# Kernel optimization log

Hardware: AMD Instinct MI355X
Metric: run time of the kernel (lower is better)

Reference implementation:

```python
import jax, jax.numpy as jnp
import numpy as np
from jax import lax

B, C, O, K, L, W = 32, 128, 128, 3, 4096, 1
PAD, DIL = 1, 1


def _conv(x, w, b):
    # x: [B,C,H,W], w: [O,C,K,1] -> [B,O,H,W] (zeros padding, stride 1)
    y = lax.conv_general_dilated(x, w, window_strides=(1, 1),
                                 padding=[(PAD, PAD), (0, 0)],
                                 rhs_dilation=(DIL, 1),
                                 dimension_numbers=('NCHW', 'OIHW', 'NCHW'))
    return y + b[None, :, None, None]


def setup_inputs() -> dict:
    key = jax.random.key(0)
    ks = jax.random.split(key, 6)
    x = jax.random.normal(ks[0], (B, C, L, W), dtype=jnp.float32)
    # offset/modulator convs are zero-init in torch; use small random values to
    # exercise the deformable gather path (represents a trained state)
    w_off = jax.random.normal(ks[1], (2 * K, C, K, 1), dtype=jnp.float32) * 0.01
    b_off = jax.random.normal(ks[2], (2 * K,), dtype=jnp.float32) * 0.1
    w_mod = jax.random.normal(ks[3], (K, C, K, 1), dtype=jnp.float32) * 0.01
    b_mod = jax.random.normal(ks[4], (K,), dtype=jnp.float32) * 0.1
    w_reg = jax.random.normal(ks[5], (O, C, K, 1), dtype=jnp.float32) * (1.0 / np.sqrt(C * K))
    return {"x": x, "w_off": w_off, "b_off": b_off,
            "w_mod": w_mod, "b_mod": b_mod, "w_reg": w_reg}


def reference(x, w_off, b_off, w_mod, b_mod, w_reg):
    b, c, h, w = x.shape
    max_offset = max(h, w) / 4.0
    offset = jnp.clip(_conv(x, w_off, b_off), -max_offset, max_offset)  # [B,2K,H,W]
    mask = 2.0 * jax.nn.sigmoid(_conv(x, w_mod, b_mod))                 # [B,K,H,W]

    off = offset.reshape(b, K, 2, h, w)
    off_y, off_x = off[:, :, 0], off[:, :, 1]                           # [B,K,H,W]

    # sampling positions (stride=1, pad_w=0, kw=1)
    base_y = (-PAD + jnp.arange(K, dtype=jnp.float32)[:, None] * DIL
              + jnp.arange(h, dtype=jnp.float32)[None, :])              # [K,H]
    py = base_y[None, :, :, None] + off_y                               # [B,K,H,W]
    px = jnp.arange(w, dtype=jnp.float32)[None, None, None, :] + off_x  # [B,K,H,W]

    y0 = jnp.floor(py); x0 = jnp.floor(px)
    iy0 = y0.astype(jnp.int32); ix0 = x0.astype(jnp.int32)
    wy1 = py - y0; wy0 = 1.0 - wy1
    wx1 = px - x0; wx0 = 1.0 - wx1

    def gather(iy, ix):
        iyc = jnp.clip(iy, 0, h - 1)
        ixc = jnp.clip(ix, 0, w - 1)
        # per-batch gather: xb [C,H,W], idx [K,H,W] -> [C,K,H,W]
        return jax.vmap(lambda xb, yb, xb_i: xb[:, yb, xb_i])(x, iyc, ixc)

    acc = jnp.zeros((b, c, K, h, w), dtype=x.dtype)
    corners = [(iy0, ix0, wy0 * wx0), (iy0, ix0 + 1, wy0 * wx1),
               (iy0 + 1, ix0, wy1 * wx0), (iy0 + 1, ix0 + 1, wy1 * wx1)]
    for iy, ix, wgt in corners:
        valid = ((iy >= 0) & (iy < h) & (ix >= 0) & (ix < w)).astype(x.dtype)
        acc = acc + gather(iy, ix) * (wgt * valid)[:, None]  # [B,C,K,H,W]

    val = acc * mask[:, None]                                 # modulated samples
    out = jnp.einsum('bckhw,ock->bohw', val, w_reg[:, :, :, 0])
    return out
```

## Files before the change

kernel.cpp:

```cpp
#include <hip/hip_runtime.h>
#include <hip/hip_bf16.h>
#include <math.h>


typedef __attribute__((ext_vector_type(8))) short bf16x8;
typedef __attribute__((ext_vector_type(4))) float f32x4;
typedef float f32x2u __attribute__((ext_vector_type(2), aligned(4)));

#define WIN 160
#define WPAD 161

static __device__ inline unsigned short f2bf(float f) {
    __hip_bfloat16 h = __float2bfloat16(f);
    union { __hip_bfloat16 b; unsigned short u; } cv;
    cv.b = h;
    return cv.u;
}

__global__ __launch_bounds__(256) void k_wra(const float* __restrict__ w_reg,
                                             const float* __restrict__ w_off,
                                             const float* __restrict__ w_mod,
                                             unsigned short* __restrict__ WrA,
                                             unsigned short* __restrict__ WcA) {
    int t = blockIdx.x * 256 + threadIdx.x;
    if (t < 49152) {
        int e  = t & 7;
        int l  = (t >> 3) & 63;
        int ms = t >> 9;
        int m  = ms / 12;
        int s  = ms - m * 12;
        int o  = m * 16 + (l & 15);
        int kc = s * 32 + ((l >> 4) & 3) * 8 + e;
        int tap = kc >> 7;
        int c   = kc & 127;
        WrA[t] = f2bf(w_reg[(o * 128 + c) * 3 + tap]);
    } else if (t < 49152 + 6144) {
        int u = t - 49152;
        int e = u & 7;
        int l = (u >> 3) & 63;
        int s = u >> 9;
        int o = l & 15;
        int c   = (s & 3) * 32 + ((l >> 4) & 3) * 8 + e;
        int tap = s >> 2;
        float v = 0.f;
        if (o < 6)      v = w_off[(o * 128 + c) * 3 + tap];
        else if (o < 9) v = w_mod[((o - 6) * 128 + c) * 3 + tap];
        WcA[u] = f2bf(v);
    }
}

__global__ __launch_bounds__(512) void k_prepm(const unsigned short* __restrict__ WcA,
                                               const float* __restrict__ x,
                                               const float* __restrict__ b_off,
                                               const float* __restrict__ b_mod,
                                               int* __restrict__ addr2,
                                               float* __restrict__ wae,
                                               float* __restrict__ wbe) {
    __shared__ float win[32 * WPAD];
    __shared__ float convx[9 * 132];
    int t = threadIdx.x;
    int l = t & 63;
    int w = t >> 6;
    int b  = blockIdx.y;
    int ib = blockIdx.x;
    int q  = l >> 4;
    int il = l & 15;
    int i0t = ib * 128;
    int wsod = i0t - 16;
    if (wsod > 4096 - WIN) wsod = 4096 - WIN;
    if (wsod < 0) wsod = 0;
    const float* xb = x + (size_t)b * 524288;
    const bf16x8* Ac = (const bf16x8*)WcA;
    int gi = i0t + w * 16 + il;

    f32x4 cv = (f32x4){0.f, 0.f, 0.f, 0.f};

    for (int cc = 0; cc < 4; ++cc) {
        int cb = cc * 32;
        __syncthreads();
#pragma unroll
        for (int it = 0; it < 3; ++it) {
            int idx = it * 512 + t;
            if (idx < 1280) {
                int r  = idx / 40;
                int cp = idx - r * 40;
                float4 v = *(const float4*)(xb + (size_t)(cb + r) * 4096 + wsod + cp * 4);
                float* dst = &win[r * WPAD + cp * 4];
                dst[0] = v.x; dst[1] = v.y; dst[2] = v.z; dst[3] = v.w;
            }
        }
        __syncthreads();

#pragma unroll
        for (int tap = 0; tap < 3; ++tap) {
            int s  = tap * 4 + cc;
            int gk = gi + tap - 1;
            bool ok = (gk >= 0) && (gk < 4096);
            int pos = gk - wsod;
            float vv[8];
#pragma unroll
            for (int e = 0; e < 8; ++e)
                vv[e] = ok ? win[(q * 8 + e) * WPAD + pos] : 0.f;
            bf16x8 Bv;
#pragma unroll
            for (int e = 0; e < 8; ++e) Bv[e] = (short)f2bf(vv[e]);
            cv = __builtin_amdgcn_mfma_f32_16x16x32_bf16(Ac[s * 64 + l], Bv, cv, 0, 0, 0);
        }
    }

    int ilocal = w * 16 + il;
#pragma unroll
    for (int rr = 0; rr < 4; ++rr) {
        int ch = q * 4 + rr;
        if (ch < 9) convx[ch * 132 + ilocal] = cv[rr];
    }
    __syncthreads();

    if (q != 0) return;
    float c9[9];
#pragma unroll
    for (int z = 0; z < 9; ++z) c9[z] = convx[z * 132 + ilocal];

#pragma unroll
    for (int k = 0; k < 3; ++k) {
        float offy = c9[2 * k]     + b_off[2 * k];
        float offx = c9[2 * k + 1] + b_off[2 * k + 1];
        offy = fminf(fmaxf(offy, -1024.f), 1024.f);
        offx = fminf(fmaxf(offx, -1024.f), 1024.f);
        float am = c9[6 + k] + b_mod[k];
        float m  = 2.f / (1.f + expf(-am));

        float py = (float)(gi - 1 + k) + offy;
        float y0 = floorf(py);
        int   iy0 = (int)y0;
        float wy1 = py - y0, wy0 = 1.f - wy1;
        float x0f = floorf(offx);
        int   ix0 = (int)x0f;
        float wx1 = offx - x0f, wx0 = 1.f - wx1;

        float sx = (ix0 == 0) ? wx0 : ((ix0 == -1) ? wx1 : 0.f);
        float scal = m * sx;

        float wAv = (iy0 >= 0 && iy0 < 4096)  ? scal * wy0 : 0.f;
        float wBv = (iy0 >= -1 && iy0 < 4095) ? scal * wy1 : 0.f;

        int addr = min(max(iy0, 0), 4094);
        bool eq = (iy0 == addr);
        float wa = eq ? wAv : (iy0 == -1   ? wBv : 0.f);
        float wb = eq ? wBv : (iy0 == 4095 ? wAv : 0.f);

        int j = (b * 3 + k) * 4096 + gi;
        addr2[j] = addr;
        wae[j] = wa;
        wbe[j] = wb;
    }
}

__global__ __launch_bounds__(512) void k_fused(const unsigned short* __restrict__ WrA,
                                               const float* __restrict__ x,
                                               const int* __restrict__ addr2,
                                               const float* __restrict__ wae,
                                               const float* __restrict__ wbe,
                                               float* __restrict__ out) {
    __shared__ float win[32 * WPAD];
    __shared__ short Bl[8][3][512];
    int t = threadIdx.x;
    int l = t & 63;
    int w = t >> 6;
    int b  = blockIdx.y;
    int ib = blockIdx.x;
    int q = l >> 4;
    int il = l & 15;
    int i0t = ib * 128;
    int i0p = i0t + w * 16 + il;
    int wsod = i0t - 16;
    if (wsod > 4096 - WIN) wsod = 4096 - WIN;
    if (wsod < 0) wsod = 0;
    const float* xb = x + (size_t)b * 524288;
    const bf16x8* Ag = (const bf16x8*)WrA;

    int   a_[3];
    float wa_[3], wb_[3];
    bool  okw[3];
#pragma unroll
    for (int k = 0; k < 3; ++k) {
        int j = (b * 3 + k) * 4096 + i0p;
        int a = addr2[j];
        a_[k]  = a;
        wa_[k] = wae[j];
        wb_[k] = wbe[j];
        okw[k] = (bool)__all(a >= wsod && a <= wsod + WIN - 2);
    }

    f32x4 acc[8];
#pragma unroll
    for (int f = 0; f < 8; ++f) acc[f] = (f32x4){0.f, 0.f, 0.f, 0.f};

#pragma unroll
    for (int it = 0; it < 3; ++it) {
        int idx = it * 512 + t;
        if (idx < 1280) {
            int r  = idx / 40;
            int cp = idx - r * 40;
            float4 v = *(const float4*)(xb + (size_t)r * 4096 + wsod + cp * 4);
            float* dst = &win[r * WPAD + cp * 4];
            dst[0] = v.x; dst[1] = v.y; dst[2] = v.z; dst[3] = v.w;
        }
    }
    __syncthreads();

    for (int cc = 0; cc < 4; ++cc) {
        int cb = cc * 32;

        bf16x8 Areg[3];
#pragma unroll
        for (int k = 0; k < 3; ++k)
            Areg[k] = Ag[(w * 12 + k * 4 + cc) * 64 + l];

#pragma unroll
        for (int k = 0; k < 3; ++k) {
            float v[8];
            float wa = wa_[k], wb = wb_[k];
            if (okw[k]) {
                int pos = a_[k] - wsod;
#pragma unroll
                for (int e = 0; e < 8; ++e) {
                    const float* base = &win[(q * 8 + e) * WPAD + pos];
                    v[e] = wa * base[0] + wb * base[1];
                }
            } else {
                int a = a_[k];
#pragma unroll
                for (int e = 0; e < 8; ++e) {
                    const float* row = xb + (size_t)(cb + q * 8 + e) * 4096;
                    f32x2u p2 = *(const f32x2u*)(row + a);
                    v[e] = wa * p2.x + wb * p2.y;
                }
            }
            bf16x8 Bv;
#pragma unroll
            for (int e = 0; e < 8; ++e) Bv[e] = (short)f2bf(v[e]);
            *(bf16x8*)&Bl[w][k][l * 8] = Bv;
        }

        float4 stg[3];
        if (cc < 3) {
            const float* src = xb + (size_t)(cb + 32) * 4096;
#pragma unroll
            for (int it = 0; it < 3; ++it) {
                int idx = it * 512 + t;
                if (idx < 1280) {
                    int r  = idx / 40;
                    int cp = idx - r * 40;
                    stg[it] = *(const float4*)(src + (size_t)r * 4096 + wsod + cp * 4);
                }
            }
        }
        __syncthreads();

        __builtin_amdgcn_s_setprio(1);
#pragma unroll
        for (int f = 0; f < 8; ++f) {
#pragma unroll
            for (int k = 0; k < 3; ++k) {
                bf16x8 Bv = *(const bf16x8*)&Bl[f][k][l * 8];
                acc[f] = __builtin_amdgcn_mfma_f32_16x16x32_bf16(Areg[k], Bv, acc[f], 0, 0, 0);
            }
        }
        __builtin_amdgcn_s_setprio(0);

        if (cc < 3) {
#pragma unroll
            for (int it = 0; it < 3; ++it) {
                int idx = it * 512 + t;
                if (idx < 1280) {
                    int r  = idx / 40;
                    int cp = idx - r * 40;
                    float* dst = &win[r * WPAD + cp * 4];
                    dst[0] = stg[it].x; dst[1] = stg[it].y;
                    dst[2] = stg[it].z; dst[3] = stg[it].w;
                }
            }
            __syncthreads();
        }
    }

    int r0 = q * 4;
#pragma unroll
    for (int f = 0; f < 8; ++f) {
#pragma unroll
        for (int r = 0; r < 4; ++r) {
            int o = w * 16 + r0 + r;
            out[((size_t)(b * 128 + o)) * 4096 + i0t + f * 16 + il] = acc[f][r];
        }
    }
}

extern "C" void kernel_launch(void* const* d_in, const int* in_sizes, int n_in,
                              void* d_out, int out_size, void* d_ws, size_t ws_size,
                              hipStream_t stream) {
    const float* x     = (const float*)d_in[0];
    const float* w_off = (const float*)d_in[1];
    const float* b_off = (const float*)d_in[2];
    const float* w_mod = (const float*)d_in[3];
    const float* b_mod = (const float*)d_in[4];
    const float* w_reg = (const float*)d_in[5];
    float* out = (float*)d_out;

    char* ws = (char*)d_ws;
    unsigned short* WrA = (unsigned short*)(ws);
    unsigned short* WcA = (unsigned short*)(ws + 98304);
    int*   addr2 = (int*)  (ws + 131072);
    float* wae   = (float*)(ws + 1703936);
    float* wbe   = (float*)(ws + 3276800);

    k_wra<<<216, 256, 0, stream>>>(w_reg, w_off, w_mod, WrA, WcA);
    k_prepm<<<dim3(32, 32), 512, 0, stream>>>(WcA, x, b_off, b_mod,
                                              addr2, wae, wbe);
    k_fused<<<dim3(32, 32), 512, 0, stream>>>(WrA, x, addr2, wae, wbe, out);
}
```

Measured before the change: 69.67 us.

## Fuse offset/mask prep kernel into main deformable conv kernel

Merges the offset/modulator convolution kernel and the sampling/GEMM kernel into one launch, so the per-position address and bilinear weights stay in registers instead of going through global workspace buffers. This removes one kernel launch and the global write and read of the addr/weight arrays. The convx scratch now aliases the Bl shared buffer, which needs an extra barrier. All lanes compute the sampling parameters redundantly instead of only one quarter of them.

```diff
diff --git a/kernel.cpp b/kernel.cpp
--- a/kernel.cpp
+++ b/kernel.cpp
@@ -49,15 +49,16 @@
     }
 }
 
-__global__ __launch_bounds__(512) void k_prepm(const unsigned short* __restrict__ WcA,
-                                               const float* __restrict__ x,
-                                               const float* __restrict__ b_off,
-                                               const float* __restrict__ b_mod,
-                                               int* __restrict__ addr2,
-                                               float* __restrict__ wae,
-                                               float* __restrict__ wbe) {
+__global__ __launch_bounds__(512) void k_all(const unsigned short* __restrict__ WrA,
+                                             const unsigned short* __restrict__ WcA,
+                                             const float* __restrict__ x,
+                                             const float* __restrict__ b_off,
+                                             const float* __restrict__ b_mod,
+                                             float* __restrict__ out) {
     __shared__ float win[32 * WPAD];
-    __shared__ float convx[9 * 132];
+    __shared__ short Bl[8][3][512];
+    float* convx = (float*)&Bl[0][0][0];
+
     int t = threadIdx.x;
     int l = t & 63;
     int w = t >> 6;
@@ -70,11 +71,11 @@
     if (wsod > 4096 - WIN) wsod = 4096 - WIN;
     if (wsod < 0) wsod = 0;
     const float* xb = x + (size_t)b * 524288;
+    const bf16x8* Ag = (const bf16x8*)WrA;
     const bf16x8* Ac = (const bf16x8*)WcA;
     int gi = i0t + w * 16 + il;
 
     f32x4 cv = (f32x4){0.f, 0.f, 0.f, 0.f};
-
     for (int cc = 0; cc < 4; ++cc) {
         int cb = cc * 32;
         __syncthreads();
@@ -96,7 +97,7 @@
             int s  = tap * 4 + cc;
             int gk = gi + tap - 1;
             bool ok = (gk >= 0) && (gk < 4096);
-            int pos = gk - wsod;
+            int pos = max(gk - wsod, 0);
             float vv[8];
 #pragma unroll
             for (int e = 0; e < 8; ++e)
@@ -115,12 +116,14 @@
         if (ch < 9) convx[ch * 132 + ilocal] = cv[rr];
     }
     __syncthreads();
-
-    if (q != 0) return;
     float c9[9];
 #pragma unroll
     for (int z = 0; z < 9; ++z) c9[z] = convx[z * 132 + ilocal];
-
+    __syncthreads();
+
+    int   a_[3];
+    float wa_[3], wb_[3];
+    bool  okw[3];
 #pragma unroll
     for (int k = 0; k < 3; ++k) {
         float offy = c9[2 * k]     + b_off[2 * k];
@@ -146,50 +149,10 @@
 
         int addr = min(max(iy0, 0), 4094);
         bool eq = (iy0 == addr);
-        float wa = eq ? wAv : (iy0 == -1   ? wBv : 0.f);
-        float wb = eq ? wBv : (iy0 == 4095 ? wAv : 0.f);
-
-        int j = (b * 3 + k) * 4096 + gi;
-        addr2[j] = addr;
-        wae[j] = wa;
-        wbe[j] = wb;
-    }
-}
-
-__global__ __launch_bounds__(512) void k_fused(const unsigned short* __restrict__ WrA,
-                                               const float* __restrict__ x,
-                                               const int* __restrict__ addr2,
-                                               const float* __restrict__ wae,
-                                               const float* __restrict__ wbe,
-                                               float* __restrict__ out) {
-    __shared__ float win[32 * WPAD];
-    __shared__ short Bl[8][3][512];
-    int t = threadIdx.x;
-    int l = t & 63;
-    int w = t >> 6;
-    int b  = blockIdx.y;
-    int ib = blockIdx.x;
-    int q = l >> 4;
-    int il = l & 15;
-    int i0t = ib * 128;
-    int i0p = i0t + w * 16 + il;
-    int wsod = i0t - 16;
-    if (wsod > 4096 - WIN) wsod = 4096 - WIN;
-    if (wsod < 0) wsod = 0;
-    const float* xb = x + (size_t)b * 524288;
-    const bf16x8* Ag = (const bf16x8*)WrA;
-
-    int   a_[3];
-    float wa_[3], wb_[3];
-    bool  okw[3];
-#pragma unroll
-    for (int k = 0; k < 3; ++k) {
-        int j = (b * 3 + k) * 4096 + i0p;
-        int a = addr2[j];
-        a_[k]  = a;
-        wa_[k] = wae[j];
-        wb_[k] = wbe[j];
-        okw[k] = (bool)__all(a >= wsod && a <= wsod + WIN - 2);
+        wa_[k] = eq ? wAv : (iy0 == -1   ? wBv : 0.f);
+        wb_[k] = eq ? wBv : (iy0 == 4095 ? wAv : 0.f);
+        a_[k]  = addr;
+        okw[k] = (bool)__all(addr >= wsod && addr <= wsod + WIN - 2);
     }
 
     f32x4 acc[8];
@@ -310,12 +273,7 @@
     char* ws = (char*)d_ws;
     unsigned short* WrA = (unsigned short*)(ws);
     unsigned short* WcA = (unsigned short*)(ws + 98304);
-    int*   addr2 = (int*)  (ws + 131072);
-    float* wae   = (float*)(ws + 1703936);
-    float* wbe   = (float*)(ws + 3276800);
 
     k_wra<<<216, 256, 0, stream>>>(w_reg, w_off, w_mod, WrA, WcA);
-    k_prepm<<<dim3(32, 32), 512, 0, stream>>>(WcA, x, b_off, b_mod,
-                                              addr2, wae, wbe);
-    k_fused<<<dim3(32, 32), 512, 0, stream>>>(WrA, x, addr2, wae, wbe, out);
-}
+    k_all<<<dim3(32, 32), 512, 0, stream>>>(WrA, WcA, x, b_off, b_mod, out);
+}
```

After: 97.43 us. 1.4x slower.
